# Kernel tuning notes

Measured on AMD Instinct MI355X. Metric: run time of the kernel, lower is better.

The kernel has to match this reference:

```python
import jax, jax.numpy as jnp
import numpy as np

B, L, C, H, W = 1, 16, 32, 64, 64
HID = C // 2


def setup_inputs() -> dict:
    key = jax.random.key(0)
    ks = jax.random.split(key, 6)
    flows = jax.random.normal(ks[0], (B, L, 2, H, W), jnp.float32) * 0.05
    images = jax.random.normal(ks[1], (B, L, C, H, W), jnp.float32)
    w1 = jax.random.normal(ks[2], (HID, 2 * C), jnp.float32) * 0.05
    b1 = jax.random.normal(ks[3], (HID,), jnp.float32) * 0.05
    w2 = jax.random.normal(ks[4], (2, HID), jnp.float32) * 0.05
    b2 = jax.random.normal(ks[5], (2,), jnp.float32) * 0.01
    decay_log = jnp.asarray(-2.0, jnp.float32)
    return dict(flows=flows, images=images, decay_log=decay_log,
                w1=w1, b1=b1, w2=w2, b2=b2)


def _bilinear_sample(img, grid):
    # img: [C,H,W]; grid: [H,W,2] with (x,y) in [-1,1]; matches torch
    # grid_sample(mode='bilinear', padding_mode='zeros', align_corners=False)
    Cv, Hv, Wv = img.shape
    gx, gy = grid[..., 0], grid[..., 1]
    ix = ((gx + 1.0) * Wv - 1.0) * 0.5
    iy = ((gy + 1.0) * Hv - 1.0) * 0.5
    ix0 = jnp.floor(ix)
    iy0 = jnp.floor(iy)
    ix1, iy1 = ix0 + 1.0, iy0 + 1.0
    wx1 = ix - ix0
    wy1 = iy - iy0
    wx0 = 1.0 - wx1
    wy0 = 1.0 - wy1

    def corner(xi, yi, w):
        valid = (xi >= 0) & (xi < Wv) & (yi >= 0) & (yi < Hv)
        xc = jnp.clip(xi, 0, Wv - 1).astype(jnp.int32)
        yc = jnp.clip(yi, 0, Hv - 1).astype(jnp.int32)
        v = img[:, yc, xc]  # [C,H,W]
        return v * (w * valid.astype(img.dtype))[None]

    return (corner(ix0, iy0, wx0 * wy0) + corner(ix1, iy0, wx1 * wy0) +
            corner(ix0, iy1, wx0 * wy1) + corner(ix1, iy1, wx1 * wy1))


def _forward(flows, images, decay_log, w1, b1, w2, b2):
    Bv, Lv, Cv, Hv, Wv = images.shape
    cum = jnp.cumsum(flows, axis=1)                      # [B,L,2,H,W]
    rel = cum[:, :, None] - cum[:, None, :]              # [B,Lt,Lk,2,H,W]
    # residual 1x1 conv stack on concat(img_t, img_k)
    img_t = jnp.broadcast_to(images[:, :, None], (Bv, Lv, Lv, Cv, Hv, Wv))
    img_k = jnp.broadcast_to(images[:, None, :], (Bv, Lv, Lv, Cv, Hv, Wv))
    feat = jnp.concatenate([img_t, img_k], axis=3)       # [B,Lt,Lk,2C,H,W]
    h = jax.nn.relu(jnp.einsum('btkchw,oc->btkohw', feat, w1)
                    + b1[None, None, None, :, None, None])
    res = (jnp.einsum('btkohw,po->btkphw', h, w2)
           + b2[None, None, None, :, None, None])        # [B,Lt,Lk,2,H,W]
    rel = rel + res
    # base grid: pixel centers in [-1,1] (align_corners=False convention)
    gy = jnp.linspace(-1.0 + 1.0 / Hv, 1.0 - 1.0 / Hv, Hv, dtype=images.dtype)
    gx = jnp.linspace(-1.0 + 1.0 / Wv, 1.0 - 1.0 / Wv, Wv, dtype=images.dtype)
    base = jnp.stack(jnp.meshgrid(gx, gy, indexing='xy'), axis=-1)  # [H,W,2]
    grid = base + jnp.moveaxis(rel, 3, -1)               # [B,Lt,Lk,H,W,2]
    wrapped_x = jnp.mod(grid[..., 0] + 1.0, 2.0) - 1.0   # wrap x into [-1,1)
    grid = jnp.stack([wrapped_x, grid[..., 1]], axis=-1)
    # sample images[b,k] at grid[b,t,k] for all (t,k) pairs
    samp = jax.vmap(                                      # over batch
        jax.vmap(                                         # over t (grid only)
            jax.vmap(_bilinear_sample, (0, 0)),           # over k
            (None, 0)),
        (0, 0))(images, grid)                             # [B,Lt,Lk,C,H,W]
    # causal decay weights: exp(-exp(decay_log)*(t-k)) for k<=t, else 0
    tk = jnp.arange(Lv)[:, None] - jnp.arange(Lv)[None, :]
    wts = jnp.where(tk >= 0,
                    jnp.exp(-jnp.exp(decay_log) * tk.astype(images.dtype)),
                    jnp.zeros((), images.dtype))
    return jnp.einsum('btkchw,tk->btchw', samp, wts)


def reference(flows, images, decay_log, w1, b1, w2, b2):
    return _forward(flows, images, decay_log, w1, b1, w2, b2)
```

## Files before the change

### kernel.cpp

```cpp
#include <hip/hip_runtime.h>

#define LL 16
#define CC 32
#define HIDN 16
#define HH 64
#define WW 64
#define HW 4096
#define NPAIR 136
#define NCHUNK 40

#define CUM_OFF  0
#define U_OFF    (LL * 2 * HW)
#define V_OFF    (U_OFF + LL * HIDN * HW)
#define DISP_OFF (V_OFF + LL * HIDN * HW)
#define IMGC_OFF (DISP_OFF + NPAIR * HW * 2)
#define A_OFF    (IMGC_OFF + LL * CC * HW / 2)

__device__ const int T_PAIR[NPAIR] = {
    0, 1,1, 2,2,2, 3,3,3,3, 4,4,4,4,4, 5,5,5,5,5,5,
    6,6,6,6,6,6,6, 7,7,7,7,7,7,7,7,
    8,8,8,8,8,8,8,8,8, 9,9,9,9,9,9,9,9,9,9,
    10,10,10,10,10,10,10,10,10,10,10,
    11,11,11,11,11,11,11,11,11,11,11,11,
    12,12,12,12,12,12,12,12,12,12,12,12,12,
    13,13,13,13,13,13,13,13,13,13,13,13,13,13,
    14,14,14,14,14,14,14,14,14,14,14,14,14,14,14,
    15,15,15,15,15,15,15,15,15,15,15,15,15,15,15,15 };
__device__ const int K_PAIR[NPAIR] = {
    0, 0,1, 0,1,2, 0,1,2,3, 0,1,2,3,4, 0,1,2,3,4,5,
    0,1,2,3,4,5,6, 0,1,2,3,4,5,6,7,
    0,1,2,3,4,5,6,7,8, 0,1,2,3,4,5,6,7,8,9,
    0,1,2,3,4,5,6,7,8,9,10,
    0,1,2,3,4,5,6,7,8,9,10,11,
    0,1,2,3,4,5,6,7,8,9,10,11,12,
    0,1,2,3,4,5,6,7,8,9,10,11,12,13,
    0,1,2,3,4,5,6,7,8,9,10,11,12,13,14,
    0,1,2,3,4,5,6,7,8,9,10,11,12,13,14,15 };
__device__ const int TRI[LL] = {0,1,3,6,10,15,21,28,36,45,55,66,78,91,105,120};

__device__ const int T_SORT[NCHUNK] = {
    0,1,2,3,4,5,6,7,8,9,10,11,12,13,14,15,
    4,5,6,7,8,9,10,11,12,13,14,15,
    8,9,10,11,12,13,14,15,
    12,13,14,15 };
__device__ const int KC_SORT[NCHUNK] = {
    0,0,0,0,0,0,0,0,0,0,0,0,0,0,0,0,
    1,1,1,1,1,1,1,1,1,1,1,1,
    2,2,2,2,2,2,2,2,
    3,3,3,3 };
__device__ const int SEG[4]  = {0, 16, 28, 36};
__device__ const int TMIN[4] = {0, 4, 8, 12};

__device__ inline unsigned short f2bf(float f) {
    unsigned u = __float_as_uint(f);
    unsigned r = (u + 0x7fffu + ((u >> 16) & 1u)) >> 16;
    return (unsigned short)r;
}
__device__ inline float bflo(unsigned u) { return __uint_as_float(u << 16); }
__device__ inline float bfhi(unsigned u) { return __uint_as_float(u & 0xffff0000u); }

__global__ __launch_bounds__(256) void cumsum_kernel(const float* __restrict__ flows,
                                                     float* __restrict__ cum) {
    int idx = blockIdx.x * 256 + threadIdx.x;
    float acc = 0.0f;
#pragma unroll
    for (int l = 0; l < LL; ++l) {
        acc += flows[l * 2 * HW + idx];
        cum[l * 2 * HW + idx] = acc;
    }
}

__global__ __launch_bounds__(256) void prep_kernel(const float* __restrict__ images,
                                                   const float* __restrict__ w1,
                                                   const float* __restrict__ b1,
                                                   float* __restrict__ ws) {
    __shared__ float w1s[HIDN * 2 * CC];
    const int tid = threadIdx.x;
    ((float4*)w1s)[tid] = ((const float4*)w1)[tid];
    __syncthreads();

    const int l  = blockIdx.y;
    const int px = blockIdx.x * 256 + tid;
    const float* img = images + (size_t)l * CC * HW;

    float x[CC];
#pragma unroll
    for (int c = 0; c < CC; ++c) x[c] = img[c * HW + px];

    float u[HIDN], v[HIDN];
#pragma unroll
    for (int o = 0; o < HIDN; ++o) { u[o] = 0.0f; v[o] = b1[o]; }
#pragma unroll
    for (int c = 0; c < CC; ++c) {
#pragma unroll
        for (int o = 0; o < HIDN; ++o) {
            u[o] = fmaf(w1s[o * 64 + c],      x[c], u[o]);
            v[o] = fmaf(w1s[o * 64 + CC + c], x[c], v[o]);
        }
    }

    float* Up = ws + U_OFF + (size_t)l * HIDN * HW + px;
    float* Vp = ws + V_OFF + (size_t)l * HIDN * HW + px;
#pragma unroll
    for (int o = 0; o < HIDN; ++o) {
        Up[o * HW] = u[o];
        Vp[o * HW] = v[o];
    }

    uint4* img4 = (uint4*)(ws + IMGC_OFF);
#pragma unroll
    for (int cg = 0; cg < 4; ++cg) {
        const int c0 = cg * 8;
        unsigned d[4];
#pragma unroll
        for (int q = 0; q < 4; ++q)
            d[q] = (unsigned)f2bf(x[c0 + 2 * q]) | ((unsigned)f2bf(x[c0 + 2 * q + 1]) << 16);
        img4[((size_t)(l * 4 + cg)) * HW + px] = make_uint4(d[0], d[1], d[2], d[3]);
    }
}

__global__ __launch_bounds__(256) void disp_kernel(float* __restrict__ ws,
                                                   const float* __restrict__ w2,
                                                   const float* __restrict__ b2) {
    __shared__ float w2s[2 * HIDN];
    __shared__ float b2s2[2];
    const int tid = threadIdx.x;
    if (tid < 2 * HIDN) w2s[tid] = w2[tid];
    if (tid < 2)        b2s2[tid] = b2[tid];
    __syncthreads();

    const int pair = blockIdx.y;
    const int t = T_PAIR[pair];
    const int k = K_PAIR[pair];
    const int px = blockIdx.x * 256 + tid;

    const float* cum = ws + CUM_OFF;
    const float* up  = ws + U_OFF + (size_t)t * HIDN * HW + px;
    const float* vp  = ws + V_OFF + (size_t)k * HIDN * HW + px;

    float res0 = b2s2[0], res1 = b2s2[1];
#pragma unroll
    for (int o = 0; o < HIDN; ++o) {
        float h = fmaxf(up[o * HW] + vp[o * HW], 0.0f);
        res0 = fmaf(w2s[o],        h, res0);
        res1 = fmaf(w2s[HIDN + o], h, res1);
    }

    float dx = (cum[(t * 2)     * HW + px] - cum[(k * 2)     * HW + px]) + res0;
    float dy = (cum[(t * 2 + 1) * HW + px] - cum[(k * 2 + 1) * HW + px]) + res1;

    ((float2*)(ws + DISP_OFF))[(size_t)pair * HW + px] = make_float2(dx, dy);
}

__global__ __launch_bounds__(256, 2) void sample_kernel(const float* __restrict__ ws_in,
                                                        float* __restrict__ ws_out,
                                                        const float* __restrict__ decay_log) {
    const int tid = threadIdx.x;
    const int hwb = blockIdx.x;
    const int s   = (hwb & 7) * 320 + (hwb >> 3);
    const int cid = s >> 6;
    const int strip = s & 63;
    const int t   = T_SORT[cid];
    const int k0  = KC_SORT[cid] * 4;

    const int lane = tid & 63;
    const int cg   = tid >> 6;
    const int px   = strip * 64 + lane;

    const float2* disp2 = (const float2*)(ws_in + DISP_OFF);
    const uint4*  img4  = (const uint4*)(ws_in + IMGC_OFF);

    const float lam = expf(decay_log[0]);
    const float bgx = (float)(2 * lane  + 1) * (1.0f / 64.0f) - 1.0f;
    const float bgy = (float)(2 * strip + 1) * (1.0f / 64.0f) - 1.0f;

    float2 dd[4];
    float  wts[4];
#pragma unroll
    for (int dk = 0; dk < 4; ++dk) {
        const int k   = k0 + dk;
        const int kcl = (k <= t) ? k : t;
        dd[dk]  = disp2[(size_t)(TRI[t] + kcl) * HW + px];
        wts[dk] = (k <= t) ? expf(-lam * (float)(t - k)) : 0.0f;
    }

    int   off[4][4];
    float cwt[4][4];
#pragma unroll
    for (int dk = 0; dk < 4; ++dk) {
        float gx = bgx + dd[dk].x;
        float gy = bgy + dd[dk].y;

        float xp = gx + 1.0f;
        xp = xp - floorf(xp * 0.5f) * 2.0f;
        float gxw = xp - 1.0f;

        float ix = ((gxw + 1.0f) * 64.0f - 1.0f) * 0.5f;
        float iy = ((gy  + 1.0f) * 64.0f - 1.0f) * 0.5f;

        float ix0f = floorf(ix), iy0f = floorf(iy);
        float fx1 = ix - ix0f, fy1 = iy - iy0f;
        float fx0 = 1.0f - fx1, fy0 = 1.0f - fy1;
        int ix0 = (int)ix0f, iy0 = (int)iy0f;
        int ix1 = ix0 + 1,   iy1 = iy0 + 1;

        int xi[4] = {ix0, ix1, ix0, ix1};
        int yi[4] = {iy0, iy0, iy1, iy1};
        float wwv[4] = {fx0 * fy0, fx1 * fy0, fx0 * fy1, fx1 * fy1};
#pragma unroll
        for (int j = 0; j < 4; ++j) {
            bool valid = (xi[j] >= 0) & (xi[j] < WW) & (yi[j] >= 0) & (yi[j] < HH);
            int xc = min(max(xi[j], 0), WW - 1);
            int yc = min(max(yi[j], 0), HH - 1);
            off[dk][j] = yc * WW + xc;
            cwt[dk][j] = valid ? wwv[j] * wts[dk] : 0.0f;
        }
    }

    uint4 q[4][4];
#pragma unroll
    for (int dk = 0; dk < 4; ++dk) {
        const size_t pb = (size_t)((k0 + dk) * 4 + cg) * HW;
#pragma unroll
        for (int j = 0; j < 4; ++j)
            q[dk][j] = img4[pb + off[dk][j]];
    }

    float acc[8];
#pragma unroll
    for (int j = 0; j < 8; ++j) acc[j] = 0.0f;

#pragma unroll
    for (int dk = 0; dk < 4; ++dk) {
#pragma unroll
        for (int j = 0; j < 4; ++j) {
            const float wj = cwt[dk][j];
            const uint4 v = q[dk][j];
            acc[0] = fmaf(wj, bflo(v.x), acc[0]);
            acc[1] = fmaf(wj, bfhi(v.x), acc[1]);
            acc[2] = fmaf(wj, bflo(v.y), acc[2]);
            acc[3] = fmaf(wj, bfhi(v.y), acc[3]);
            acc[4] = fmaf(wj, bflo(v.z), acc[4]);
            acc[5] = fmaf(wj, bfhi(v.z), acc[5]);
            acc[6] = fmaf(wj, bflo(v.w), acc[6]);
            acc[7] = fmaf(wj, bfhi(v.w), acc[7]);
        }
    }

    float* Ap = ws_out + A_OFF + ((size_t)cid * CC + cg * 8) * HW + px;
#pragma unroll
    for (int j = 0; j < 8; ++j) Ap[j * HW] = acc[j];
}

__global__ __launch_bounds__(256) void reduce_kernel(const float* __restrict__ ws,
                                                     float* __restrict__ out) {
    const int gid = blockIdx.x * 256 + threadIdx.x;
    const int t   = gid >> 15;
    const int c   = (gid >> 10) & 31;
    const int px4 = gid & 1023;

    const float4* A4 = (const float4*)(ws + A_OFF);
    const int n = 1 + (t >= 4) + (t >= 8) + (t >= 12);

    float4 s = make_float4(0.0f, 0.0f, 0.0f, 0.0f);
    for (int kc = 0; kc < n; ++kc) {
        int cid = SEG[kc] + (t - TMIN[kc]);
        float4 a = A4[((size_t)cid * CC + c) * (HW / 4) + px4];
        s.x += a.x; s.y += a.y; s.z += a.z; s.w += a.w;
    }
    ((float4*)out)[gid] = s;
}

extern "C" void kernel_launch(void* const* d_in, const int* in_sizes, int n_in,
                              void* d_out, int out_size, void* d_ws, size_t ws_size,
                              hipStream_t stream) {
    const float* flows     = (const float*)d_in[0];
    const float* images    = (const float*)d_in[1];
    const float* decay_log = (const float*)d_in[2];
    const float* w1        = (const float*)d_in[3];
    const float* b1        = (const float*)d_in[4];
    const float* w2        = (const float*)d_in[5];
    const float* b2        = (const float*)d_in[6];
    float* out = (float*)d_out;
    float* ws  = (float*)d_ws;

    cumsum_kernel<<<dim3(2 * HW / 256), dim3(256), 0, stream>>>(flows, ws + CUM_OFF);

    prep_kernel<<<dim3(HW / 256, LL), dim3(256), 0, stream>>>(images, w1, b1, ws);

    disp_kernel<<<dim3(HW / 256, NPAIR), dim3(256), 0, stream>>>(ws, w2, b2);

    sample_kernel<<<dim3(8 * 320), dim3(256), 0, stream>>>(ws, ws, decay_log);

    reduce_kernel<<<dim3(2048), dim3(256), 0, stream>>>(ws, out);
}
```

Measured before the change: 115.3 us.

## Fuse displacement computation into sample kernel via shared memory

Removes the separate displacement kernel and its global buffer. Each sample block now computes the four displacement vectors for its strip and k-chunk from the U/V hidden features and cumulative flows, stages them in shared memory, then samples. This saves one launch and a global write/read round trip. The cost is that padded pairs with k>t are now computed too, and each block spends extra loads and ALU work before its gather phase.

New measurement: 110.3 us. 1.05x faster.

```diff
diff --git a/kernel.cpp b/kernel.cpp
--- a/kernel.cpp
+++ b/kernel.cpp
@@ -6,37 +6,13 @@
 #define HH 64
 #define WW 64
 #define HW 4096
-#define NPAIR 136
 #define NCHUNK 40
 
 #define CUM_OFF  0
 #define U_OFF    (LL * 2 * HW)
 #define V_OFF    (U_OFF + LL * HIDN * HW)
-#define DISP_OFF (V_OFF + LL * HIDN * HW)
-#define IMGC_OFF (DISP_OFF + NPAIR * HW * 2)
+#define IMGC_OFF (V_OFF + LL * HIDN * HW)
 #define A_OFF    (IMGC_OFF + LL * CC * HW / 2)
-
-__device__ const int T_PAIR[NPAIR] = {
-    0, 1,1, 2,2,2, 3,3,3,3, 4,4,4,4,4, 5,5,5,5,5,5,
-    6,6,6,6,6,6,6, 7,7,7,7,7,7,7,7,
-    8,8,8,8,8,8,8,8,8, 9,9,9,9,9,9,9,9,9,9,
-    10,10,10,10,10,10,10,10,10,10,10,
-    11,11,11,11,11,11,11,11,11,11,11,11,
-    12,12,12,12,12,12,12,12,12,12,12,12,12,
-    13,13,13,13,13,13,13,13,13,13,13,13,13,13,
-    14,14,14,14,14,14,14,14,14,14,14,14,14,14,14,
-    15,15,15,15,15,15,15,15,15,15,15,15,15,15,15,15 };
-__device__ const int K_PAIR[NPAIR] = {
-    0, 0,1, 0,1,2, 0,1,2,3, 0,1,2,3,4, 0,1,2,3,4,5,
-    0,1,2,3,4,5,6, 0,1,2,3,4,5,6,7,
-    0,1,2,3,4,5,6,7,8, 0,1,2,3,4,5,6,7,8,9,
-    0,1,2,3,4,5,6,7,8,9,10,
-    0,1,2,3,4,5,6,7,8,9,10,11,
-    0,1,2,3,4,5,6,7,8,9,10,11,12,
-    0,1,2,3,4,5,6,7,8,9,10,11,12,13,
-    0,1,2,3,4,5,6,7,8,9,10,11,12,13,14,
-    0,1,2,3,4,5,6,7,8,9,10,11,12,13,14,15 };
-__device__ const int TRI[LL] = {0,1,3,6,10,15,21,28,36,45,55,66,78,91,105,120};
 
 __device__ const int T_SORT[NCHUNK] = {
     0,1,2,3,4,5,6,7,8,9,10,11,12,13,14,15,
@@ -119,43 +95,20 @@
     }
 }
 
-__global__ __launch_bounds__(256) void disp_kernel(float* __restrict__ ws,
-                                                   const float* __restrict__ w2,
-                                                   const float* __restrict__ b2) {
-    __shared__ float w2s[2 * HIDN];
-    __shared__ float b2s2[2];
+__global__ __launch_bounds__(256, 2) void sample_kernel(const float* __restrict__ ws_in,
+                                                        float* __restrict__ ws_out,
+                                                        const float* __restrict__ w2,
+                                                        const float* __restrict__ b2,
+                                                        const float* __restrict__ decay_log) {
+    __shared__ float  w2s[2 * HIDN];
+    __shared__ float  b2s2[2];
+    __shared__ float2 dls[4][64];
+
     const int tid = threadIdx.x;
     if (tid < 2 * HIDN) w2s[tid] = w2[tid];
     if (tid < 2)        b2s2[tid] = b2[tid];
     __syncthreads();
 
-    const int pair = blockIdx.y;
-    const int t = T_PAIR[pair];
-    const int k = K_PAIR[pair];
-    const int px = blockIdx.x * 256 + tid;
-
-    const float* cum = ws + CUM_OFF;
-    const float* up  = ws + U_OFF + (size_t)t * HIDN * HW + px;
-    const float* vp  = ws + V_OFF + (size_t)k * HIDN * HW + px;
-
-    float res0 = b2s2[0], res1 = b2s2[1];
-#pragma unroll
-    for (int o = 0; o < HIDN; ++o) {
-        float h = fmaxf(up[o * HW] + vp[o * HW], 0.0f);
-        res0 = fmaf(w2s[o],        h, res0);
-        res1 = fmaf(w2s[HIDN + o], h, res1);
-    }
-
-    float dx = (cum[(t * 2)     * HW + px] - cum[(k * 2)     * HW + px]) + res0;
-    float dy = (cum[(t * 2 + 1) * HW + px] - cum[(k * 2 + 1) * HW + px]) + res1;
-
-    ((float2*)(ws + DISP_OFF))[(size_t)pair * HW + px] = make_float2(dx, dy);
-}
-
-__global__ __launch_bounds__(256, 2) void sample_kernel(const float* __restrict__ ws_in,
-                                                        float* __restrict__ ws_out,
-                                                        const float* __restrict__ decay_log) {
-    const int tid = threadIdx.x;
     const int hwb = blockIdx.x;
     const int s   = (hwb & 7) * 320 + (hwb >> 3);
     const int cid = s >> 6;
@@ -163,33 +116,52 @@
     const int t   = T_SORT[cid];
     const int k0  = KC_SORT[cid] * 4;
 
+    const float* cum = ws_in + CUM_OFF;
+    const float* Ub  = ws_in + U_OFF;
+    const float* Vb  = ws_in + V_OFF;
+    const uint4* img4 = (const uint4*)(ws_in + IMGC_OFF);
+
+    {
+        const int kk  = tid >> 6;
+        const int lp  = tid & 63;
+        const int px1 = strip * 64 + lp;
+        const int k1  = k0 + kk;
+
+        const float* up = Ub + (size_t)t  * HIDN * HW + px1;
+        const float* vp = Vb + (size_t)k1 * HIDN * HW + px1;
+
+        float res0 = b2s2[0], res1 = b2s2[1];
+#pragma unroll
+        for (int o = 0; o < HIDN; ++o) {
+            float h = fmaxf(up[o * HW] + vp[o * HW], 0.0f);
+            res0 = fmaf(w2s[o],        h, res0);
+            res1 = fmaf(w2s[HIDN + o], h, res1);
+        }
+
+        float dx = (cum[(t * 2)     * HW + px1] - cum[(k1 * 2)     * HW + px1]) + res0;
+        float dy = (cum[(t * 2 + 1) * HW + px1] - cum[(k1 * 2 + 1) * HW + px1]) + res1;
+        dls[kk][lp] = make_float2(dx, dy);
+    }
+    __syncthreads();
+
     const int lane = tid & 63;
     const int cg   = tid >> 6;
     const int px   = strip * 64 + lane;
 
-    const float2* disp2 = (const float2*)(ws_in + DISP_OFF);
-    const uint4*  img4  = (const uint4*)(ws_in + IMGC_OFF);
-
     const float lam = expf(decay_log[0]);
     const float bgx = (float)(2 * lane  + 1) * (1.0f / 64.0f) - 1.0f;
     const float bgy = (float)(2 * strip + 1) * (1.0f / 64.0f) - 1.0f;
 
-    float2 dd[4];
-    float  wts[4];
-#pragma unroll
-    for (int dk = 0; dk < 4; ++dk) {
-        const int k   = k0 + dk;
-        const int kcl = (k <= t) ? k : t;
-        dd[dk]  = disp2[(size_t)(TRI[t] + kcl) * HW + px];
-        wts[dk] = (k <= t) ? expf(-lam * (float)(t - k)) : 0.0f;
-    }
-
     int   off[4][4];
     float cwt[4][4];
 #pragma unroll
     for (int dk = 0; dk < 4; ++dk) {
-        float gx = bgx + dd[dk].x;
-        float gy = bgy + dd[dk].y;
+        const int k = k0 + dk;
+        const float wtd = (k <= t) ? expf(-lam * (float)(t - k)) : 0.0f;
+        float2 d = dls[dk][lane];
+
+        float gx = bgx + d.x;
+        float gy = bgy + d.y;
 
         float xp = gx + 1.0f;
         xp = xp - floorf(xp * 0.5f) * 2.0f;
@@ -213,7 +185,7 @@
             int xc = min(max(xi[j], 0), WW - 1);
             int yc = min(max(yi[j], 0), HH - 1);
             off[dk][j] = yc * WW + xc;
-            cwt[dk][j] = valid ? wwv[j] * wts[dk] : 0.0f;
+            cwt[dk][j] = valid ? wwv[j] * wtd : 0.0f;
         }
     }
 
@@ -288,9 +260,7 @@
 
     prep_kernel<<<dim3(HW / 256, LL), dim3(256), 0, stream>>>(images, w1, b1, ws);
 
-    disp_kernel<<<dim3(HW / 256, NPAIR), dim3(256), 0, stream>>>(ws, w2, b2);
-
-    sample_kernel<<<dim3(8 * 320), dim3(256), 0, stream>>>(ws, ws, decay_log);
+    sample_kernel<<<dim3(8 * 320), dim3(256), 0, stream>>>(ws, ws, w2, b2, decay_log);
 
     reduce_kernel<<<dim3(2048), dim3(256), 0, stream>>>(ws, out);
 }
```
